# Kernel optimization log

Hardware: AMD Instinct MI355X
Metric: run time of the kernel (lower is better)

Reference implementation:

```python
import jax, jax.numpy as jnp
import numpy as np

HIDDEN = 1024
NUM_HEADS = 16
HEAD_DIM = HIDDEN // NUM_HEADS
B, S = 4, 4096


def setup_inputs() -> dict:
    key = jax.random.key(0)
    ks = jax.random.split(key, 7)
    scale = 1.0 / np.sqrt(HIDDEN)
    return {
        "hidden_states": jax.random.normal(ks[0], (B, S, HIDDEN), dtype=jnp.float32),
        "Wq": jax.random.normal(ks[1], (HIDDEN, HIDDEN), dtype=jnp.float32) * scale,
        "bq": jax.random.normal(ks[2], (HIDDEN,), dtype=jnp.float32) * 0.01,
        "Wk": jax.random.normal(ks[3], (HIDDEN, HIDDEN), dtype=jnp.float32) * scale,
        "bk": jax.random.normal(ks[4], (HIDDEN,), dtype=jnp.float32) * 0.01,
        "Wv": jax.random.normal(ks[5], (HIDDEN, HIDDEN), dtype=jnp.float32) * scale,
        "bv": jax.random.normal(ks[6], (HIDDEN,), dtype=jnp.float32) * 0.01,
    }


def _split_heads(x):
    # [B, S, H*D] -> [B, H, S, D]
    b, s, _ = x.shape
    return x.reshape(b, s, NUM_HEADS, HEAD_DIM).transpose(0, 2, 1, 3)


def reference(hidden_states, Wq, bq, Wk, bk, Wv, bv):
    # Fused-style QKV: single stacked GEMM, then split + reshape to heads.
    Wqkv = jnp.concatenate([Wq, Wk, Wv], axis=1)          # [H, 3H]
    bqkv = jnp.concatenate([bq, bk, bv], axis=0)           # [3H]
    qkv = jnp.einsum("bsh,hf->bsf", hidden_states, Wqkv) + bqkv  # [B, S, 3H]
    q, k, v = jnp.split(qkv, 3, axis=-1)
    return (_split_heads(q), _split_heads(k), _split_heads(v))
```

## Files before the change

kernel.cpp:

```cpp
#include <hip/hip_runtime.h>
#include <hip/hip_bf16.h>


#define M_TOT 16384
#define N_TOT 3072
#define K_TOT 1024

typedef __bf16 bf16x8 __attribute__((ext_vector_type(8)));
typedef float f32x16 __attribute__((ext_vector_type(16)));

#define AS1(p) ((const __attribute__((address_space(1))) void*)(p))
#define AS3(p) ((__attribute__((address_space(3))) void*)(p))

__device__ __forceinline__ unsigned short f2bf(float f) {
    unsigned int u = __builtin_bit_cast(unsigned int, f);
    u += 0x7fffu + ((u >> 16) & 1u);
    return (unsigned short)(u >> 16);
}

__global__ void convert_hidden(const float* __restrict__ x,
                               unsigned short* __restrict__ y, int n4) {
    int i = blockIdx.x * blockDim.x + threadIdx.x;
    int stride = gridDim.x * blockDim.x;
    for (; i < n4; i += stride) {
        float4 v = ((const float4*)x)[i];
        ushort4 o;
        o.x = f2bf(v.x); o.y = f2bf(v.y); o.z = f2bf(v.z); o.w = f2bf(v.w);
        ((ushort4*)y)[i] = o;
    }
}

__global__ void convert_weights(const float* __restrict__ Wq,
                                const float* __restrict__ Wk,
                                const float* __restrict__ Wv,
                                unsigned short* __restrict__ Bt) {
    __shared__ unsigned short tile[64][65];
    const float* W = (blockIdx.z == 0) ? Wq : (blockIdx.z == 1) ? Wk : Wv;
    int k0 = blockIdx.y * 64;
    int f0 = blockIdx.x * 64;
    int tx = threadIdx.x & 63;
    int ty = threadIdx.x >> 6;
#pragma unroll
    for (int r = 0; r < 16; ++r) {
        int k = ty + r * 4;
        tile[k][tx] = f2bf(W[(size_t)(k0 + k) * 1024 + f0 + tx]);
    }
    __syncthreads();
#pragma unroll
    for (int r = 0; r < 16; ++r) {
        int fr = ty + r * 4;
        Bt[(size_t)(blockIdx.z * 1024 + f0 + fr) * 1024 + k0 + tx] = tile[tx][fr];
    }
}

__launch_bounds__(512, 2)
__global__ void qkv_gemm(const unsigned short* __restrict__ A,
                         const unsigned short* __restrict__ Bt,
                         const float* __restrict__ bq,
                         const float* __restrict__ bk,
                         const float* __restrict__ bv,
                         float* __restrict__ out) {
    __shared__ __align__(16) unsigned short As[2][16384];
    __shared__ __align__(16) unsigned short Bs[2][16384];

    const int tid  = threadIdx.x;
    const int wave = tid >> 6;
    const int lane = tid & 63;
    const int r5   = lane & 31;
    const int half = lane >> 5;

    const int orig = blockIdx.x;
    const int wg   = (orig & 7) * 96 + (orig >> 3);
    const int bm   = wg & 63;
    const int bn   = wg >> 6;

    const int wr = wave >> 2;
    const int wc = wave & 3;

    f32x16 acc[4][2] = {};

    const int trow = tid >> 3;
    const int tkq8 = ((tid & 7) ^ (trow & 7)) * 8;
    const unsigned short* gA = A  + (size_t)(bm * 256 + trow) * 1024 + tkq8;
    const unsigned short* gB = Bt + (size_t)(bn * 256 + trow) * 1024 + tkq8;

#define STAGE(i, koff, dstA, dstB)                                              \
    do {                                                                        \
        __builtin_amdgcn_global_load_lds(                                       \
            AS1(gA + (size_t)(i)*65536 + (koff)),                               \
            AS3((dstA) + ((i)*512 + wave * 64) * 8), 16, 0, 0);                 \
        __builtin_amdgcn_global_load_lds(                                       \
            AS1(gB + (size_t)(i)*65536 + (koff)),                               \
            AS3((dstB) + ((i)*512 + wave * 64) * 8), 16, 0, 0);                 \
    } while (0)

#pragma unroll
    for (int i = 0; i < 4; ++i) STAGE(i, 0, As[0], Bs[0]);

#pragma unroll 2
    for (int t = 0; t < 16; ++t) {
        const int cur = t & 1;
        const int nxt = cur ^ 1;
        const bool pf = (t < 15);
        const int koff = (t + 1) * 64;
        const unsigned short* Ab = As[cur];
        const unsigned short* Bb = Bs[cur];

#pragma unroll
        for (int ks = 0; ks < 4; ++ks) {
            bf16x8 av[4], bvv[2];
            const int prd = ((ks * 2 + half) ^ (r5 & 7)) * 8;
            if (ks == 0) {
                if (pf) STAGE(0, koff, As[nxt], Bs[nxt]);
                if (pf) asm volatile("s_waitcnt vmcnt(2)" ::: "memory");
                else    asm volatile("s_waitcnt vmcnt(0)" ::: "memory");
                __builtin_amdgcn_s_barrier();
                __builtin_amdgcn_sched_barrier(0);
#pragma unroll
                for (int ib = 0; ib < 4; ++ib)
                    av[ib] = *(const bf16x8*)&Ab[(wr * 128 + ib * 32 + r5) * 64 + prd];
#pragma unroll
                for (int jb = 0; jb < 2; ++jb)
                    bvv[jb] = *(const bf16x8*)&Bb[(wc * 64 + jb * 32 + r5) * 64 + prd];
            } else {
#pragma unroll
                for (int ib = 0; ib < 4; ++ib)
                    av[ib] = *(const bf16x8*)&Ab[(wr * 128 + ib * 32 + r5) * 64 + prd];
#pragma unroll
                for (int jb = 0; jb < 2; ++jb)
                    bvv[jb] = *(const bf16x8*)&Bb[(wc * 64 + jb * 32 + r5) * 64 + prd];
                if (pf) STAGE(ks, koff, As[nxt], Bs[nxt]);
                __builtin_amdgcn_s_barrier();
            }
            asm volatile("s_waitcnt lgkmcnt(0)" ::: "memory");
            __builtin_amdgcn_sched_barrier(0);
            __builtin_amdgcn_s_setprio(1);
#pragma unroll
            for (int ib = 0; ib < 4; ++ib)
#pragma unroll
                for (int jb = 0; jb < 2; ++jb)
                    acc[ib][jb] = __builtin_amdgcn_mfma_f32_32x32x16_bf16(
                        av[ib], bvv[jb], acc[ib][jb], 0, 0, 0);
            __builtin_amdgcn_s_setprio(0);
            __builtin_amdgcn_s_barrier();
        }
    }
#undef STAGE

    const int section = bn >> 2;
    const int nloc0   = (bn & 3) * 256 + wc * 64;
    const float* bias = (section == 0) ? bq : (section == 1) ? bk : bv;
    float* outsec = out + (size_t)section * (4u * 16u * 4096u * 64u);

#pragma unroll
    for (int jb = 0; jb < 2; ++jb) {
        int f = nloc0 + jb * 32 + r5;
        float bval = bias[f];
        int h = f >> 6, d = f & 63;
        size_t hb = (size_t)h * (4096u * 64u);
#pragma unroll
        for (int ib = 0; ib < 4; ++ib) {
            int mbase = bm * 256 + wr * 128 + ib * 32 + 4 * half;
#pragma unroll
            for (int reg = 0; reg < 16; ++reg) {
                int m = mbase + (reg & 3) + 8 * (reg >> 2);
                int b = m >> 12, s = m & 4095;
                outsec[(size_t)b * (16u * 4096u * 64u) + hb + (size_t)s * 64u + d] =
                    acc[ib][jb][reg] + bval;
            }
        }
    }
}

extern "C" void kernel_launch(void* const* d_in, const int* in_sizes, int n_in,
                              void* d_out, int out_size, void* d_ws, size_t ws_size,
                              hipStream_t stream) {
    const float* hs = (const float*)d_in[0];
    const float* Wq = (const float*)d_in[1];
    const float* bq = (const float*)d_in[2];
    const float* Wk = (const float*)d_in[3];
    const float* bk = (const float*)d_in[4];
    const float* Wv = (const float*)d_in[5];
    const float* bv = (const float*)d_in[6];
    float* out = (float*)d_out;

    unsigned short* Abf  = (unsigned short*)d_ws;
    unsigned short* Btbf = Abf + (size_t)M_TOT * K_TOT;

    convert_hidden<<<2048, 256, 0, stream>>>(hs, Abf, (M_TOT * K_TOT) / 4);
    convert_weights<<<dim3(16, 16, 3), 256, 0, stream>>>(Wq, Wk, Wv, Btbf);
    qkv_gemm<<<dim3((M_TOT / 256) * (N_TOT / 256)), 512, 0, stream>>>(Abf, Btbf, bq, bk, bv, out);
}
```

Baseline: 389.9 us.

## Make GEMM persistent over three tiles with cross-tile prefetch

The launch shrinks to 256 workgroups and each one computes three 256x256 output tiles in sequence. The first K-chunk of the next tile is prefetched during the last iteration of the current tile, so the pipeline does not drain between tiles. The tile-to-XCD mapping is changed and one of the per-k-step barriers is removed. The epilogue stores now run serially inside each workgroup and are no longer overlapped with other workgroups' compute, and fewer workgroups may leave some CUs idle.

New measurement: 372.1 us. -4.6%, faster.

```diff
diff --git a/kernel.cpp b/kernel.cpp
--- a/kernel.cpp
+++ b/kernel.cpp
@@ -68,108 +68,139 @@
     const int lane = tid & 63;
     const int r5   = lane & 31;
     const int half = lane >> 5;
-
-    const int orig = blockIdx.x;
-    const int wg   = (orig & 7) * 96 + (orig >> 3);
-    const int bm   = wg & 63;
-    const int bn   = wg >> 6;
+    const int swr  = r5 & 7;
+
+    const int xcd = blockIdx.x & 7;
+    const int j   = blockIdx.x >> 3;
+    const int jm  = j & 7;
+    const int jn  = j >> 3;
 
     const int wr = wave >> 2;
     const int wc = wave & 3;
 
-    f32x16 acc[4][2] = {};
-
     const int trow = tid >> 3;
     const int tkq8 = ((tid & 7) ^ (trow & 7)) * 8;
+
+    int st = xcd * 3;
+    int bm = (st & 7) * 8 + jm;
+    int bn = (st >> 3) * 4 + jn;
     const unsigned short* gA = A  + (size_t)(bm * 256 + trow) * 1024 + tkq8;
     const unsigned short* gB = Bt + (size_t)(bn * 256 + trow) * 1024 + tkq8;
 
-#define STAGE(i, koff, dstA, dstB)                                              \
+#define STAGE(c)                                                                \
     do {                                                                        \
-        __builtin_amdgcn_global_load_lds(                                       \
-            AS1(gA + (size_t)(i)*65536 + (koff)),                               \
-            AS3((dstA) + ((i)*512 + wave * 64) * 8), 16, 0, 0);                 \
-        __builtin_amdgcn_global_load_lds(                                       \
-            AS1(gB + (size_t)(i)*65536 + (koff)),                               \
-            AS3((dstB) + ((i)*512 + wave * 64) * 8), 16, 0, 0);                 \
+        __builtin_amdgcn_global_load_lds(AS1(sA + (size_t)(c)*65536),           \
+                                         AS3(dA + ((c)*512 + wave * 64) * 8),   \
+                                         16, 0, 0);                             \
+        __builtin_amdgcn_global_load_lds(AS1(sB + (size_t)(c)*65536),           \
+                                         AS3(dB + ((c)*512 + wave * 64) * 8),   \
+                                         16, 0, 0);                             \
     } while (0)
 
-#pragma unroll
-    for (int i = 0; i < 4; ++i) STAGE(i, 0, As[0], Bs[0]);
+    {
+        const unsigned short* sA = gA;
+        const unsigned short* sB = gB;
+        unsigned short* dA = (unsigned short*)As[0];
+        unsigned short* dB = (unsigned short*)Bs[0];
+#pragma unroll
+        for (int c = 0; c < 4; ++c) STAGE(c);
+    }
+
+    for (int i = 0; i < 3; ++i) {
+        int bm2 = bm, bn2 = bn;
+        const unsigned short *gA2 = gA, *gB2 = gB;
+        if (i < 2) {
+            int st2 = xcd * 3 + i + 1;
+            bm2 = (st2 & 7) * 8 + jm;
+            bn2 = (st2 >> 3) * 4 + jn;
+            gA2 = A  + (size_t)(bm2 * 256 + trow) * 1024 + tkq8;
+            gB2 = Bt + (size_t)(bn2 * 256 + trow) * 1024 + tkq8;
+        }
+
+        f32x16 acc[4][2] = {};
 
 #pragma unroll 2
-    for (int t = 0; t < 16; ++t) {
-        const int cur = t & 1;
-        const int nxt = cur ^ 1;
-        const bool pf = (t < 15);
-        const int koff = (t + 1) * 64;
-        const unsigned short* Ab = As[cur];
-        const unsigned short* Bb = Bs[cur];
-
-#pragma unroll
-        for (int ks = 0; ks < 4; ++ks) {
-            bf16x8 av[4], bvv[2];
-            const int prd = ((ks * 2 + half) ^ (r5 & 7)) * 8;
-            if (ks == 0) {
-                if (pf) STAGE(0, koff, As[nxt], Bs[nxt]);
-                if (pf) asm volatile("s_waitcnt vmcnt(2)" ::: "memory");
-                else    asm volatile("s_waitcnt vmcnt(0)" ::: "memory");
-                __builtin_amdgcn_s_barrier();
+        for (int t = 0; t < 16; ++t) {
+            const int cur = t & 1;
+            const unsigned short* Ab = As[cur];
+            const unsigned short* Bb = Bs[cur];
+            unsigned short* dA = (unsigned short*)As[cur ^ 1];
+            unsigned short* dB = (unsigned short*)Bs[cur ^ 1];
+            const bool stg = (t < 15) || (i < 2);
+            const unsigned short* sA = (t < 15) ? gA + (size_t)(t + 1) * 64 : gA2;
+            const unsigned short* sB = (t < 15) ? gB + (size_t)(t + 1) * 64 : gB2;
+
+#pragma unroll
+            for (int ks = 0; ks < 4; ++ks) {
+                bf16x8 av[4], bvv[2];
+                const int prd = ((ks * 2 + half) ^ swr) * 8;
+                if (ks == 0) {
+                    if (stg) {
+                        STAGE(0);
+                        asm volatile("s_waitcnt vmcnt(2)" ::: "memory");
+                    } else {
+                        asm volatile("s_waitcnt vmcnt(0)" ::: "memory");
+                    }
+                    __builtin_amdgcn_s_barrier();
+                    __builtin_amdgcn_sched_barrier(0);
+#pragma unroll
+                    for (int ib = 0; ib < 4; ++ib)
+                        av[ib] = *(const bf16x8*)&Ab[(wr * 128 + ib * 32 + r5) * 64 + prd];
+#pragma unroll
+                    for (int jb = 0; jb < 2; ++jb)
+                        bvv[jb] = *(const bf16x8*)&Bb[(wc * 64 + jb * 32 + r5) * 64 + prd];
+                } else {
+#pragma unroll
+                    for (int ib = 0; ib < 4; ++ib)
+                        av[ib] = *(const bf16x8*)&Ab[(wr * 128 + ib * 32 + r5) * 64 + prd];
+#pragma unroll
+                    for (int jb = 0; jb < 2; ++jb)
+                        bvv[jb] = *(const bf16x8*)&Bb[(wc * 64 + jb * 32 + r5) * 64 + prd];
+                    if (stg) STAGE(ks);
+                }
+                asm volatile("s_waitcnt lgkmcnt(0)" ::: "memory");
                 __builtin_amdgcn_sched_barrier(0);
+                __builtin_amdgcn_s_setprio(1);
 #pragma unroll
                 for (int ib = 0; ib < 4; ++ib)
-                    av[ib] = *(const bf16x8*)&Ab[(wr * 128 + ib * 32 + r5) * 64 + prd];
-#pragma unroll
-                for (int jb = 0; jb < 2; ++jb)
-                    bvv[jb] = *(const bf16x8*)&Bb[(wc * 64 + jb * 32 + r5) * 64 + prd];
-            } else {
-#pragma unroll
-                for (int ib = 0; ib < 4; ++ib)
-                    av[ib] = *(const bf16x8*)&Ab[(wr * 128 + ib * 32 + r5) * 64 + prd];
-#pragma unroll
-                for (int jb = 0; jb < 2; ++jb)
-                    bvv[jb] = *(const bf16x8*)&Bb[(wc * 64 + jb * 32 + r5) * 64 + prd];
-                if (pf) STAGE(ks, koff, As[nxt], Bs[nxt]);
-                __builtin_amdgcn_s_barrier();
+#pragma unroll
+                    for (int jb = 0; jb < 2; ++jb)
+                        acc[ib][jb] = __builtin_amdgcn_mfma_f32_32x32x16_bf16(
+                            av[ib], bvv[jb], acc[ib][jb], 0, 0, 0);
+                __builtin_amdgcn_s_setprio(0);
             }
-            asm volatile("s_waitcnt lgkmcnt(0)" ::: "memory");
-            __builtin_amdgcn_sched_barrier(0);
-            __builtin_amdgcn_s_setprio(1);
-#pragma unroll
-            for (int ib = 0; ib < 4; ++ib)
-#pragma unroll
-                for (int jb = 0; jb < 2; ++jb)
-                    acc[ib][jb] = __builtin_amdgcn_mfma_f32_32x32x16_bf16(
-                        av[ib], bvv[jb], acc[ib][jb], 0, 0, 0);
-            __builtin_amdgcn_s_setprio(0);
             __builtin_amdgcn_s_barrier();
         }
-    }
-#undef STAGE
-
-    const int section = bn >> 2;
-    const int nloc0   = (bn & 3) * 256 + wc * 64;
-    const float* bias = (section == 0) ? bq : (section == 1) ? bk : bv;
-    float* outsec = out + (size_t)section * (4u * 16u * 4096u * 64u);
-
-#pragma unroll
-    for (int jb = 0; jb < 2; ++jb) {
-        int f = nloc0 + jb * 32 + r5;
-        float bval = bias[f];
-        int h = f >> 6, d = f & 63;
-        size_t hb = (size_t)h * (4096u * 64u);
-#pragma unroll
-        for (int ib = 0; ib < 4; ++ib) {
-            int mbase = bm * 256 + wr * 128 + ib * 32 + 4 * half;
-#pragma unroll
-            for (int reg = 0; reg < 16; ++reg) {
-                int m = mbase + (reg & 3) + 8 * (reg >> 2);
-                int b = m >> 12, s = m & 4095;
-                outsec[(size_t)b * (16u * 4096u * 64u) + hb + (size_t)s * 64u + d] =
-                    acc[ib][jb][reg] + bval;
+
+        {
+            const int section = bn >> 2;
+            const int nloc0   = (bn & 3) * 256 + wc * 64;
+            const float* bias = (section == 0) ? bq : (section == 1) ? bk : bv;
+            float* outsec = out + (size_t)section * (4u * 16u * 4096u * 64u);
+
+#pragma unroll
+            for (int jb = 0; jb < 2; ++jb) {
+                int f = nloc0 + jb * 32 + r5;
+                float bval = bias[f];
+                int h = f >> 6, d = f & 63;
+                size_t hb = (size_t)h * (4096u * 64u);
+#pragma unroll
+                for (int ib = 0; ib < 4; ++ib) {
+                    int mbase = bm * 256 + wr * 128 + ib * 32 + 4 * half;
+#pragma unroll
+                    for (int reg = 0; reg < 16; ++reg) {
+                        int m = mbase + (reg & 3) + 8 * (reg >> 2);
+                        int b = m >> 12, s = m & 4095;
+                        outsec[(size_t)b * (16u * 4096u * 64u) + hb + (size_t)s * 64u + d] =
+                            acc[ib][jb][reg] + bval;
+                    }
+                }
             }
         }
-    }
+
+        bm = bm2; bn = bn2; gA = gA2; gB = gB2;
+    }
+#undef STAGE
 }
 
 extern "C" void kernel_launch(void* const* d_in, const int* in_sizes, int n_in,
@@ -189,5 +220,5 @@
 
     convert_hidden<<<2048, 256, 0, stream>>>(hs, Abf, (M_TOT * K_TOT) / 4);
     convert_weights<<<dim3(16, 16, 3), 256, 0, stream>>>(Wq, Wk, Wv, Btbf);
-    qkv_gemm<<<dim3((M_TOT / 256) * (N_TOT / 256)), 512, 0, stream>>>(Abf, Btbf, bq, bk, bv, out);
-}
+    qkv_gemm<<<256, 512, 0, stream>>>(Abf, Btbf, bq, bk, bv, out);
+}
```
